# Optimization experiments

Hardware: AMD Instinct MI355X
Metric: run time of the kernel (lower is better)

The kernel has to match this reference:

```python
import jax, jax.numpy as jnp
import numpy as np

EPS = 1e-5

def conv3x3(x, w, b=None):
    # NCHW, OIHW, stride 1, padding 1
    y = jax.lax.conv_general_dilated(x, w, (1, 1), ((1, 1), (1, 1)),
                                     dimension_numbers=('NCHW', 'OIHW', 'NCHW'))
    if b is not None:
        y = y + b[None, :, None, None]
    return y

def batchnorm(x, g, b):
    # training-mode BN (PyTorch default): biased variance over (N,H,W)
    m = x.mean((0, 2, 3), keepdims=True)
    v = x.var((0, 2, 3), keepdims=True)
    return (x - m) * jax.lax.rsqrt(v + EPS) * g[None, :, None, None] + b[None, :, None, None]

def upsample2x_align_corners(x):
    # bilinear, align_corners=True, scale_factor=2
    def lerp_axis(a, Lin, axis):
        Lout = 2 * Lin
        c = jnp.arange(Lout, dtype=a.dtype) * (Lin - 1) / (Lout - 1)
        i0 = jnp.floor(c).astype(jnp.int32)
        i1 = jnp.minimum(i0 + 1, Lin - 1)
        w = c - i0.astype(a.dtype)
        shape = [1] * a.ndim
        shape[axis] = Lout
        w = w.reshape(shape)
        return jnp.take(a, i0, axis=axis) * (1 - w) + jnp.take(a, i1, axis=axis) * w
    x = lerp_axis(x, x.shape[2], 2)
    x = lerp_axis(x, x.shape[3], 3)
    return x

def deform_sample(x, offsets):
    # torchvision DeformConv2d v1 sampling: kernel 3x3, pad 1, offsets [B,18,H,W]
    # layout: per kernel point k (row-major), channels (2k, 2k+1) = (dy, dx)
    B, C, H, W = x.shape
    K = 9
    off = offsets.reshape(B, K, 2, H, W)
    ky, kx = jnp.meshgrid(jnp.arange(3) - 1, jnp.arange(3) - 1, indexing='ij')
    ky = ky.reshape(K).astype(x.dtype)
    kx = kx.reshape(K).astype(x.dtype)
    gy = jnp.arange(H, dtype=x.dtype)[None, None, :, None]
    gx = jnp.arange(W, dtype=x.dtype)[None, None, None, :]
    py = gy + ky[None, :, None, None] + off[:, :, 0]  # [B,K,H,W]
    px = gx + kx[None, :, None, None] + off[:, :, 1]
    y0 = jnp.floor(py)
    x0 = jnp.floor(px)
    wy = (py - y0)[:, None]  # [B,1,K,H,W]
    wx = (px - x0)[:, None]
    y0i = y0.astype(jnp.int32)
    x0i = x0.astype(jnp.int32)
    x_flat = x.reshape(B, C, H * W)
    def gather(yi, xi):
        valid = ((yi >= 0) & (yi < H) & (xi >= 0) & (xi < W))
        idx = jnp.clip(yi, 0, H - 1) * W + jnp.clip(xi, 0, W - 1)  # [B,K,H,W]
        g = jnp.take_along_axis(x_flat, idx.reshape(B, 1, K * H * W), axis=2)
        return g.reshape(B, C, K, H, W) * valid[:, None].astype(x.dtype)
    v00 = gather(y0i, x0i)
    v01 = gather(y0i, x0i + 1)
    v10 = gather(y0i + 1, x0i)
    v11 = gather(y0i + 1, x0i + 1)
    return (v00 * (1 - wy) * (1 - wx) + v01 * (1 - wy) * wx
            + v10 * wy * (1 - wx) + v11 * wy * wx)

def setup_inputs() -> dict:
    key = jax.random.key(0)
    ks = jax.random.split(key, 6)
    B, in_ch, skip_ch, out_ch = 4, 256, 128, 128
    Hs, Ws = 128, 128
    x = jax.random.normal(ks[0], (B, in_ch, Hs // 2, Ws // 2), jnp.float32)
    skip = jax.random.normal(ks[1], (B, skip_ch, Hs, Ws), jnp.float32)
    cat_ch = in_ch + skip_ch
    conv1_w = jax.random.normal(ks[2], (out_ch, cat_ch, 3, 3), jnp.float32) * (2.0 / (cat_ch * 9)) ** 0.5
    off_w = jax.random.normal(ks[3], (18, out_ch, 3, 3), jnp.float32) * 0.01
    off_b = jnp.zeros((18,), jnp.float32)
    def_w = jax.random.normal(ks[4], (out_ch, out_ch, 3, 3), jnp.float32) * (2.0 / (out_ch * 9)) ** 0.5
    def_b = jnp.zeros((out_ch,), jnp.float32)
    return {
        'x': x, 'skip': skip,
        'conv1_w': conv1_w,
        'bn1_g': jnp.ones((out_ch,), jnp.float32), 'bn1_b': jnp.zeros((out_ch,), jnp.float32),
        'off_w': off_w, 'off_b': off_b,
        'def_w': def_w, 'def_b': def_b,
        'bn2_g': jnp.ones((out_ch,), jnp.float32), 'bn2_b': jnp.zeros((out_ch,), jnp.float32),
    }

def reference(x, skip, conv1_w, bn1_g, bn1_b, off_w, off_b, def_w, def_b, bn2_g, bn2_b):
    xu = upsample2x_align_corners(x)
    dh = skip.shape[2] - xu.shape[2]
    dw = skip.shape[3] - xu.shape[3]
    if dh != 0 or dw != 0:
        xu = jnp.pad(xu, ((0, 0), (0, 0), (dh // 2, dh - dh // 2), (dw // 2, dw - dw // 2)))
    cat = jnp.concatenate([skip, xu], axis=1)
    h = jax.nn.relu(batchnorm(conv3x3(cat, conv1_w), bn1_g, bn1_b))
    offsets = conv3x3(h, off_w, off_b)  # [B,18,H,W]
    sampled = deform_sample(h, offsets)  # [B,C,9,H,W]
    O = def_w.shape[0]
    y = jnp.einsum('ock,bckhw->bohw', def_w.reshape(O, def_w.shape[1], 9), sampled)
    y = y + def_b[None, :, None, None]
    return jax.nn.relu(batchnorm(y, bn2_g, bn2_b))
```

## Files before the change

### kernel.cpp

```cpp
#include <hip/hip_runtime.h>
#include <hip/hip_bf16.h>

typedef __hip_bfloat16 bf16;
typedef __bf16 bf16x8 __attribute__((ext_vector_type(8)));
typedef __bf16 bf16x4 __attribute__((ext_vector_type(4)));
typedef float  f32x4  __attribute__((ext_vector_type(4)));

constexpr int NB   = 4;
constexpr int H    = 128;
constexpr int W    = 128;
constexpr int HW   = H * W;
constexpr int NPIX = NB * HW;
constexpr int CCAT = 384;
constexpr int CSKIP= 128;
constexpr int CIN  = 256;
constexpr int CO   = 128;
constexpr int HS   = 64;
constexpr int WP   = 130;
constexpr int K1   = 3456;
constexpr int KD   = 1152;
constexpr int NBORD= 2 * WP + 2 * (WP - 2);
constexpr float EPS = 1e-5f;

__device__ __forceinline__ float b2f(bf16 v){ return __bfloat162float(v); }
__device__ __forceinline__ bf16  f2b(float v){ return __float2bfloat16(v); }

__device__ __forceinline__ void async_copy16(const void* g, void* s){
    __builtin_amdgcn_global_load_lds((const __attribute__((address_space(1))) void*)g,
                                     (__attribute__((address_space(3))) void*)s, 16, 0, 0);
}

__device__ __forceinline__ int swizzle_row(int raw){
    return (raw & 7) * 64 + (raw >> 3);
}

__device__ __forceinline__ void border_yx(int p, int& y, int& x){
    if (p < WP)             { y = 0;        x = p; }
    else if (p < 2 * WP)    { y = WP - 1;   x = p - WP; }
    else if (p < 2 * WP + (WP - 2)) { y = p - 2 * WP + 1;          x = 0; }
    else                    { y = p - (2 * WP + (WP - 2)) + 1;     x = WP - 1; }
}

__global__ void k_prep(float* __restrict__ sums, bf16* __restrict__ catp,
                       bf16* __restrict__ hp){
    int i = blockIdx.x * blockDim.x + threadIdx.x;
    int stride = gridDim.x * blockDim.x;
    for (int j = i; j < 512; j += stride) sums[j] = 0.f;
    const int nCat = NB * NBORD * CCAT;
    for (int j = i; j < nCat; j += stride){
        int c = j % CCAT, r = j / CCAT, p = r % NBORD, b = r / NBORD;
        int y, x; border_yx(p, y, x);
        catp[(((size_t)b * WP + y) * WP + x) * CCAT + c] = f2b(0.f);
    }
    const int nHp = NB * NBORD * CO;
    for (int j = i; j < nHp; j += stride){
        int c = j % CO, r = j / CO, p = r % NBORD, b = r / NBORD;
        int y, x; border_yx(p, y, x);
        hp[(((size_t)b * WP + y) * WP + x) * CO + c] = f2b(0.f);
    }
}

__global__ __launch_bounds__(256) void k_build_cat2(const float* __restrict__ x,
                                                    const float* __restrict__ skip,
                                                    bf16* __restrict__ catp){
    constexpr int TS = 66;
    __shared__ bf16 tile[128 * TS];
    int t  = threadIdx.x;
    int y  = blockIdx.x % H, b = blockIdx.x / H;
    int xx = t & 127, cp = t >> 7;

    float cy = (y * 63.0f) / 127.0f;
    int   y0 = (int)cy;
    int   y1 = min(y0 + 1, HS - 1);
    float wy = cy - y0;
    float cxf = (xx * 63.0f) / 127.0f;
    int   x0 = (int)cxf;
    int   x1 = min(x0 + 1, HS - 1);
    float wx = cxf - x0;

    bf16* orow = catp + (((size_t)b * WP + y + 1) * WP + 1) * CCAT;

    for (int chunk = 0; chunk < 6; chunk++){
        int cbase = chunk * 64;
        if (chunk >= 1) __syncthreads();
        if (chunk < 2){
            const float* sb = skip + ((size_t)(b * CSKIP + cbase + cp * 32) * H + y) * W;
#pragma unroll
            for (int i = 0; i < 32; i++)
                tile[xx * TS + cp * 32 + i] = f2b(sb[(size_t)i * HW + xx]);
        } else {
            int icb = (chunk - 2) * 64 + cp * 32;
            const float* xr0 = x + ((size_t)(b * CIN + icb) * HS + y0) * HS;
            const float* xr1 = x + ((size_t)(b * CIN + icb) * HS + y1) * HS;
#pragma unroll
            for (int i = 0; i < 32; i++){
                const float* r0 = xr0 + (size_t)i * HS * HS;
                const float* r1 = xr1 + (size_t)i * HS * HS;
                float v0 = r0[x0] * (1 - wx) + r0[x1] * wx;
                float v1 = r1[x0] * (1 - wx) + r1[x1] * wx;
                tile[xx * TS + cp * 32 + i] = f2b(v0 * (1 - wy) + v1 * wy);
            }
        }
        __syncthreads();
        int cc2 = (t & 31) * 2;
        int px0 = t >> 5;
#pragma unroll
        for (int pp = 0; pp < 16; pp++){
            int px = pp * 8 + px0;
            unsigned int v = *(const unsigned int*)&tile[px * TS + cc2];
            *(unsigned int*)&orow[(size_t)px * CCAT + cbase + cc2] = v;
        }
    }
}

__global__ void k_tr_all(const float* __restrict__ w1, const float* __restrict__ wo,
                         const float* __restrict__ wd,
                         bf16* __restrict__ wt1, bf16* __restrict__ wto,
                         bf16* __restrict__ wtd){
    int i = blockIdx.x * blockDim.x + threadIdx.x;
    if (i < CO * K1){
        int k = i % K1, oc = i / K1;
        int ky = k / 1152, r = k % 1152, kx = r / 384, ic = r % 384;
        wt1[i] = f2b(w1[((oc * CCAT + ic) * 3 + ky) * 3 + kx]);
        return;
    }
    i -= CO * K1;
    if (i < 32 * KD){
        int kk = i % KD, o = i / KD;
        int ky = kk / 384, r = kk % 384, kx = r >> 7, ic = r & 127;
        wto[i] = (o < 18) ? f2b(wo[((o * CO + ic) * 3 + ky) * 3 + kx]) : f2b(0.f);
        return;
    }
    i -= 32 * KD;
    if (i < CO * KD){
        int kk = i % KD, o = i / KD;
        int kp = kk >> 7, c = kk & 127;
        wtd[i] = f2b(wd[(o * CO + c) * 9 + kp]);
    }
}

__global__ __launch_bounds__(256) void k_conv1_mfma(const bf16* __restrict__ catp,
                                                    const bf16* __restrict__ wbt,
                                                    bf16* __restrict__ hp,
                                                    float* __restrict__ sums){
    __shared__ unsigned short Ab[128 * 64];
    __shared__ unsigned short Bb[128 * 64];
    __shared__ float ps[256];
    int t = threadIdx.x;
    int l = t & 63, w = t >> 6;
    int row = swizzle_row(blockIdx.x);
    int y = row & 127, b = row >> 7;

    int pr   = l >> 3;
    int koct = (l & 7) ^ pr;
    int m    = l & 15, quad = l >> 4;
    int wm   = w & 1,  wn   = w >> 1;

    f32x4 acc[4][4];
#pragma unroll
    for (int i = 0; i < 4; i++)
#pragma unroll
        for (int j = 0; j < 4; j++) acc[i][j] = f32x4{0.f, 0.f, 0.f, 0.f};

    const size_t rowStride = (size_t)WP * CCAT;
    for (int ky = 0; ky < 3; ky++){
        const bf16* Arow = catp + ((size_t)(b * WP) + y + ky) * rowStride;
        for (int kc = 0; kc < 18; kc++){
            int c0 = kc / 6, r0 = (kc % 6) * 64;
            __syncthreads();
#pragma unroll
            for (int i = 0; i < 4; i++){
                int px = w * 32 + i * 8 + pr;
                async_copy16(Arow + (size_t)(px + c0) * CCAT + r0 + koct * 8,
                             &Ab[(w * 32 + i * 8) * 64]);
            }
            int kg = ky * 1152 + kc * 64;
#pragma unroll
            for (int i = 0; i < 4; i++){
                int oc = w * 32 + i * 8 + pr;
                async_copy16(wbt + (size_t)oc * K1 + kg + koct * 8,
                             &Bb[(w * 32 + i * 8) * 64]);
            }
            __syncthreads();
            const bf16x8* ap = (const bf16x8*)Ab;
            const bf16x8* bp = (const bf16x8*)Bb;
#pragma unroll
            for (int ks = 0; ks < 2; ks++){
                bf16x8 af[4], bfr[4];
#pragma unroll
                for (int mi = 0; mi < 4; mi++){
                    int px = wm * 64 + mi * 16 + m;
                    af[mi] = ap[px * 8 + ((ks * 4 + quad) ^ (px & 7))];
                }
#pragma unroll
                for (int ni = 0; ni < 4; ni++){
                    int oc = wn * 64 + ni * 16 + m;
                    bfr[ni] = bp[oc * 8 + ((ks * 4 + quad) ^ (oc & 7))];
                }
#pragma unroll
                for (int mi = 0; mi < 4; mi++)
#pragma unroll
                    for (int ni = 0; ni < 4; ni++)
                        acc[mi][ni] = __builtin_amdgcn_mfma_f32_16x16x32_bf16(
                            af[mi], bfr[ni], acc[mi][ni], 0, 0, 0);
            }
        }
    }
    size_t obase = (((size_t)b * WP + y + 1) * WP + 1) * CO;
#pragma unroll
    for (int mi = 0; mi < 4; mi++){
        int p0 = wm * 64 + mi * 16 + quad * 4;
#pragma unroll
        for (int ni = 0; ni < 4; ni++){
            int oc = wn * 64 + ni * 16 + m;
#pragma unroll
            for (int r = 0; r < 4; r++)
                hp[obase + (size_t)(p0 + r) * CO + oc] = f2b(acc[mi][ni][r]);
        }
    }
    ps[t] = 0.f;
    __syncthreads();
#pragma unroll
    for (int ni = 0; ni < 4; ni++){
        int ch = wn * 64 + ni * 16 + m;
        float s = 0.f, q = 0.f;
#pragma unroll
        for (int mi = 0; mi < 4; mi++)
#pragma unroll
            for (int r = 0; r < 4; r++){
                float v = acc[mi][ni][r];
                s += v; q += v * v;
            }
        atomicAdd(&ps[ch], s);
        atomicAdd(&ps[128 + ch], q);
    }
    __syncthreads();
    if (t < 128){
        atomicAdd(&sums[t],       ps[t]);
        atomicAdd(&sums[128 + t], ps[128 + t]);
    }
}

__global__ __launch_bounds__(256) void k_bn_apply_pad(bf16* __restrict__ t,
                                                      const float* __restrict__ sums,
                                                      const float* __restrict__ g,
                                                      const float* __restrict__ bb){
    __shared__ float ssc[256];
    int tt = threadIdx.x;
    if (tt < 128){
        float mean = sums[tt] / (float)NPIX;
        float var  = sums[128 + tt] / (float)NPIX - mean * mean;
        float scale = g[tt] * rsqrtf(var + EPS);
        ssc[tt]       = scale;
        ssc[128 + tt] = bb[tt] - mean * scale;
    }
    __syncthreads();
    int i = blockIdx.x * 256 + tt;
    if (i >= NPIX * CO) return;
    int c = i & 127;
    int pix = i >> 7;
    int xw = pix & 127, yh = (pix >> 7) & 127, b = pix >> 14;
    size_t a = (((size_t)b * WP + yh + 1) * WP + xw + 1) * CO + c;
    float v = b2f(t[a]) * ssc[c] + ssc[128 + c];
    t[a] = f2b(v > 0.f ? v : 0.f);
}

__global__ __launch_bounds__(256) void k_conv_off_mfma(const bf16* __restrict__ hp,
                                                       const bf16* __restrict__ wob,
                                                       const float* __restrict__ off_b,
                                                       bf16* __restrict__ offs){
    __shared__ unsigned short Ab[128 * 64];
    __shared__ unsigned short Bb[32 * 64];
    int t = threadIdx.x, l = t & 63, w = t >> 6;
    int row = swizzle_row(blockIdx.x);
    int y = row & 127, b = row >> 7;
    int pr = l >> 3, koct = (l & 7) ^ pr;
    int m = l & 15, quad = l >> 4;
    int wm = w & 1, wn = w >> 1;

    f32x4 acc[4];
#pragma unroll
    for (int i = 0; i < 4; i++) acc[i] = f32x4{0.f, 0.f, 0.f, 0.f};

    const size_t rowStride = (size_t)WP * CO;
    for (int ky = 0; ky < 3; ky++){
        const bf16* Arow = hp + ((size_t)(b * WP) + y + ky) * rowStride;
        for (int kc = 0; kc < 6; kc++){
            int kx = kc >> 1, r0 = (kc & 1) * 64;
            __syncthreads();
#pragma unroll
            for (int i = 0; i < 4; i++){
                int px = w * 32 + i * 8 + pr;
                async_copy16(Arow + (size_t)(px + kx) * CO + r0 + koct * 8,
                             &Ab[(w * 32 + i * 8) * 64]);
            }
            int kg = ky * 384 + kx * 128 + r0;
            async_copy16(wob + (size_t)(w * 8 + pr) * KD + kg + koct * 8,
                         &Bb[(w * 8) * 64]);
            __syncthreads();
            const bf16x8* ap = (const bf16x8*)Ab;
            const bf16x8* bp = (const bf16x8*)Bb;
#pragma unroll
            for (int ks = 0; ks < 2; ks++){
                int oc = wn * 16 + m;
                bf16x8 bfr = bp[oc * 8 + ((ks * 4 + quad) ^ (oc & 7))];
#pragma unroll
                for (int mi = 0; mi < 4; mi++){
                    int px = wm * 64 + mi * 16 + m;
                    bf16x8 af = ap[px * 8 + ((ks * 4 + quad) ^ (px & 7))];
                    acc[mi] = __builtin_amdgcn_mfma_f32_16x16x32_bf16(af, bfr, acc[mi], 0, 0, 0);
                }
            }
        }
    }
    int oc = wn * 16 + m;
    if (oc < 18){
        float bias = off_b[oc];
        int rowpix = b * HW + y * W;
#pragma unroll
        for (int mi = 0; mi < 4; mi++){
            int p0 = wm * 64 + mi * 16 + quad * 4;
#pragma unroll
            for (int r = 0; r < 4; r++)
                offs[(size_t)(rowpix + p0 + r) * 18 + oc] = f2b(acc[mi][r] + bias);
        }
    }
}

__global__ __launch_bounds__(256) void k_deform_mfma(const bf16* __restrict__ hp,
                                                     const bf16* __restrict__ offs,
                                                     const bf16* __restrict__ wdb,
                                                     const float* __restrict__ def_b,
                                                     bf16* __restrict__ y,
                                                     float* __restrict__ sums){
    __shared__ unsigned short Ab[128 * 64];
    __shared__ unsigned short Bb[128 * 64];
    __shared__ int2   sc_yx[9 * 128];
    __shared__ float4 sc_w[9 * 128];
    __shared__ float  ps[256];

    int t = threadIdx.x, l = t & 63, w = t >> 6;
    int row = swizzle_row(blockIdx.x);
    int yrow = row & 127, b = row >> 7;
    int rowpix = b * HW + yrow * W;

    for (int idx = t; idx < 9 * 128; idx += 256){
        int kp = idx >> 7, px = idx & 127;
        float dy = b2f(offs[(size_t)(rowpix + px) * 18 + 2 * kp]);
        float dx = b2f(offs[(size_t)(rowpix + px) * 18 + 2 * kp + 1]);
        float py = yrow + (kp / 3 - 1) + dy;
        float pxx = px + (kp % 3 - 1) + dx;
        float fy = floorf(py), fx = floorf(pxx);
        float wy = py - fy, wx = pxx - fx;
        int y0 = (int)fy, x0 = (int)fx;
        bool vy0 = (y0 >= 0) && (y0 < H);
        bool vy1 = (y0 + 1 >= 0) && (y0 + 1 < H);
        bool vx0 = (x0 >= 0) && (x0 < W);
        bool vx1 = (x0 + 1 >= 0) && (x0 + 1 < W);
        int y0c = min(max(y0, 0), H - 1),     y1c = min(max(y0 + 1, 0), H - 1);
        int x0c = min(max(x0, 0), W - 1),     x1c = min(max(x0 + 1, 0), W - 1);
        sc_yx[idx] = make_int2(((y0c + 1) * WP) | (((y1c + 1) * WP) << 16),
                               (x0c + 1) | ((x1c + 1) << 16));
        sc_w[idx] = make_float4((1 - wy) * (1 - wx) * (float)(vy0 && vx0),
                                (1 - wy) * wx       * (float)(vy0 && vx1),
                                wy * (1 - wx)       * (float)(vy1 && vx0),
                                wy * wx             * (float)(vy1 && vx1));
    }
    __syncthreads();

    int pr = l >> 3, koct = (l & 7) ^ pr;
    int m = l & 15, quad = l >> 4;
    int wm = w & 1, wn = w >> 1;
    int g = l >> 4, j = l & 15;

    f32x4 acc[4][4];
#pragma unroll
    for (int i = 0; i < 4; i++)
#pragma unroll
        for (int jj = 0; jj < 4; jj++) acc[i][jj] = f32x4{0.f, 0.f, 0.f, 0.f};

    const bf16* hpb = hp + (size_t)b * WP * WP * CO;

    for (int kc = 0; kc < 18; kc++){
        int kp = kc >> 1, ch = (kc & 1) * 64;
        __syncthreads();
        int kg = kp * 128 + ch;
#pragma unroll
        for (int i = 0; i < 4; i++){
            int oc = w * 32 + i * 8 + pr;
            async_copy16(wdb + (size_t)oc * KD + kg + koct * 8,
                         &Bb[(w * 32 + i * 8) * 64]);
        }
        int cb = ch + j * 4;
#pragma unroll
        for (int p = 0; p < 8; p++){
            int px = w * 32 + g * 8 + p;
            int idx = kp * 128 + px;
            int2 yx = sc_yx[idx];
            float4 w4 = sc_w[idx];
            int r0 = yx.x & 0xffff, r1 = ((unsigned)yx.x) >> 16;
            int c0 = yx.y & 0xffff, c1 = ((unsigned)yx.y) >> 16;
            const bf16* base = hpb + cb;
            bf16x4 s00 = *(const bf16x4*)(base + (size_t)(r0 + c0) * CO);
            bf16x4 s01 = *(const bf16x4*)(base + (size_t)(r0 + c1) * CO);
            bf16x4 s10 = *(const bf16x4*)(base + (size_t)(r1 + c0) * CO);
            bf16x4 s11 = *(const bf16x4*)(base + (size_t)(r1 + c1) * CO);
            bf16x4 pv;
#pragma unroll
            for (int r = 0; r < 4; r++){
                float v = w4.x * (float)s00[r] + w4.y * (float)s01[r]
                        + w4.z * (float)s10[r] + w4.w * (float)s11[r];
                pv[r] = (__bf16)v;
            }
            int oct_sw = (j >> 1) ^ (px & 7);
            *(bf16x4*)&Ab[px * 64 + oct_sw * 8 + (j & 1) * 4] = pv;
        }
        __syncthreads();
        const bf16x8* ap = (const bf16x8*)Ab;
        const bf16x8* bp = (const bf16x8*)Bb;
#pragma unroll
        for (int ks = 0; ks < 2; ks++){
            bf16x8 af[4], bfr[4];
#pragma unroll
            for (int mi = 0; mi < 4; mi++){
                int px = wm * 64 + mi * 16 + m;
                af[mi] = ap[px * 8 + ((ks * 4 + quad) ^ (px & 7))];
            }
#pragma unroll
            for (int ni = 0; ni < 4; ni++){
                int oc = wn * 64 + ni * 16 + m;
                bfr[ni] = bp[oc * 8 + ((ks * 4 + quad) ^ (oc & 7))];
            }
#pragma unroll
            for (int mi = 0; mi < 4; mi++)
#pragma unroll
                for (int ni = 0; ni < 4; ni++)
                    acc[mi][ni] = __builtin_amdgcn_mfma_f32_16x16x32_bf16(
                        af[mi], bfr[ni], acc[mi][ni], 0, 0, 0);
        }
    }
#pragma unroll
    for (int mi = 0; mi < 4; mi++){
        int p0 = wm * 64 + mi * 16 + quad * 4;
#pragma unroll
        for (int ni = 0; ni < 4; ni++){
            int oc = wn * 64 + ni * 16 + m;
            float bias = def_b[oc];
#pragma unroll
            for (int r = 0; r < 4; r++)
                y[(size_t)(rowpix + p0 + r) * CO + oc] = f2b(acc[mi][ni][r] + bias);
        }
    }
    ps[t] = 0.f;
    __syncthreads();
#pragma unroll
    for (int ni = 0; ni < 4; ni++){
        int ch = wn * 64 + ni * 16 + m;
        float bias = def_b[ch];
        float s = 0.f, q = 0.f;
#pragma unroll
        for (int mi = 0; mi < 4; mi++)
#pragma unroll
            for (int r = 0; r < 4; r++){
                float v = acc[mi][ni][r] + bias;
                s += v; q += v * v;
            }
        atomicAdd(&ps[ch], s);
        atomicAdd(&ps[128 + ch], q);
    }
    __syncthreads();
    if (t < 128){
        atomicAdd(&sums[t],       ps[t]);
        atomicAdd(&sums[128 + t], ps[128 + t]);
    }
}

__global__ __launch_bounds__(256) void k_final(const bf16* __restrict__ yb,
                                               const float* __restrict__ sums,
                                               const float* __restrict__ g,
                                               const float* __restrict__ bb,
                                               float* __restrict__ out){
    __shared__ unsigned short tile[128 * 129];
    __shared__ float ssc[256];
    int t = threadIdx.x;
    if (t < 128){
        float mean = sums[t] / (float)NPIX;
        float var  = sums[128 + t] / (float)NPIX - mean * mean;
        float scale = g[t] * rsqrtf(var + EPS);
        ssc[t]       = scale;
        ssc[128 + t] = bb[t] - mean * scale;
    }
    int yrow = blockIdx.x % H, b = blockIdx.x / H;
    int rowbase = b * HW + yrow * W;
    const unsigned short* src = (const unsigned short*)yb;
    for (int it = 0; it < 64; it++){
        int idx = it * 256 + t;
        int c = idx & 127, px = idx >> 7;
        tile[px * 129 + c] = src[(size_t)(rowbase + px) * CO + c];
    }
    __syncthreads();
    for (int it = 0; it < 64; it++){
        int idx = it * 256 + t;
        int xw = idx & 127, o = idx >> 7;
        unsigned short u = tile[xw * 129 + o];
        float v = (float)(*(const __bf16*)&u);
        v = v * ssc[o] + ssc[128 + o];
        out[(((size_t)b * CO + o) * H + yrow) * W + xw] = v > 0.f ? v : 0.f;
    }
}

extern "C" void kernel_launch(void* const* d_in, const int* in_sizes, int n_in,
                              void* d_out, int out_size, void* d_ws, size_t ws_size,
                              hipStream_t stream){
    const float* x      = (const float*)d_in[0];
    const float* skip   = (const float*)d_in[1];
    const float* conv1w = (const float*)d_in[2];
    const float* bn1g   = (const float*)d_in[3];
    const float* bn1b   = (const float*)d_in[4];
    const float* offw   = (const float*)d_in[5];
    const float* offb   = (const float*)d_in[6];
    const float* defw   = (const float*)d_in[7];
    const float* defb   = (const float*)d_in[8];
    const float* bn2g   = (const float*)d_in[9];
    const float* bn2b   = (const float*)d_in[10];
    float* out = (float*)d_out;

    char* ws = (char*)d_ws;
    size_t off_bytes = 0;
    auto alloc = [&](size_t bytes) -> void* {
        void* p = ws + off_bytes;
        off_bytes += (bytes + 255) & ~(size_t)255;
        return p;
    };
    const size_t catp_elems = (size_t)NB * WP * WP * CCAT;
    const size_t hp_elems   = (size_t)NB * WP * WP * CO;
    bf16*  catp  = (bf16*) alloc(catp_elems * 2);
    bf16*  hp    = (bf16*) alloc(hp_elems * 2);
    bf16*  offs  = (bf16*) alloc((size_t)NPIX * 18 * 2);
    bf16*  yb    = (bf16*) alloc((size_t)NPIX * CO * 2);
    bf16*  wbt   = (bf16*) alloc((size_t)CO * K1 * 2);
    bf16*  wob   = (bf16*) alloc((size_t)32 * KD * 2);
    bf16*  wdb   = (bf16*) alloc((size_t)CO * KD * 2);
    float* sums  = (float*)alloc(512 * 4);
    float* sums1 = sums;
    float* sums2 = sums + 256;

    k_prep<<<1024, 256, 0, stream>>>(sums, catp, hp);

    k_build_cat2<<<NB * H, 256, 0, stream>>>(x, skip, catp);

    const int ntr = CO * K1 + 32 * KD + CO * KD;
    k_tr_all<<<(ntr + 255) / 256, 256, 0, stream>>>(conv1w, offw, defw, wbt, wob, wdb);

    k_conv1_mfma<<<NB * H, 256, 0, stream>>>(catp, wbt, hp, sums1);

    k_bn_apply_pad<<<(NPIX * CO + 255) / 256, 256, 0, stream>>>(hp, sums1, bn1g, bn1b);

    k_conv_off_mfma<<<NB * H, 256, 0, stream>>>(hp, wob, offb, offs);

    k_deform_mfma<<<NB * H, 256, 0, stream>>>(hp, offs, wdb, defb, yb, sums2);

    k_final<<<NB * H, 256, 0, stream>>>(yb, sums2, bn2g, bn2b, out);
}
```

Before: 349.5 us.

## Process two output rows per conv1 block, drop row swizzle, shuffle-reduce BN stats

conv1 now uses 512-thread blocks that each compute two image rows (256 pixels) against a shared 128-channel weight tile. Each weight chunk is therefore loaded once for twice the pixels, and the grid is halved. The XCD-style row swizzle is removed from all kernels in favour of plain linear row mapping. BN partial sums are wave-reduced with shuffles before the LDS atomics, which cuts atomic contention. The larger LDS footprint and block size may lower occupancy, and dropping the swizzle changes cache locality across dies.

```diff
diff --git a/kernel.cpp b/kernel.cpp
--- a/kernel.cpp
+++ b/kernel.cpp
@@ -30,10 +30,6 @@
                                      (__attribute__((address_space(3))) void*)s, 16, 0, 0);
 }
 
-__device__ __forceinline__ int swizzle_row(int raw){
-    return (raw & 7) * 64 + (raw >> 3);
-}
-
 __device__ __forceinline__ void border_yx(int p, int& y, int& x){
     if (p < WP)             { y = 0;        x = p; }
     else if (p < 2 * WP)    { y = WP - 1;   x = p - WP; }
@@ -139,22 +135,21 @@
     }
 }
 
-__global__ __launch_bounds__(256) void k_conv1_mfma(const bf16* __restrict__ catp,
+__global__ __launch_bounds__(512) void k_conv1_mfma(const bf16* __restrict__ catp,
                                                     const bf16* __restrict__ wbt,
                                                     bf16* __restrict__ hp,
                                                     float* __restrict__ sums){
-    __shared__ unsigned short Ab[128 * 64];
+    __shared__ unsigned short Ab[256 * 64];
     __shared__ unsigned short Bb[128 * 64];
     __shared__ float ps[256];
     int t = threadIdx.x;
     int l = t & 63, w = t >> 6;
-    int row = swizzle_row(blockIdx.x);
-    int y = row & 127, b = row >> 7;
+    int y0 = (blockIdx.x & 63) * 2, b = blockIdx.x >> 6;
 
     int pr   = l >> 3;
     int koct = (l & 7) ^ pr;
     int m    = l & 15, quad = l >> 4;
-    int wm   = w & 1,  wn   = w >> 1;
+    int wm   = w & 3,  wn   = w >> 2;
 
     f32x4 acc[4][4];
 #pragma unroll
@@ -163,23 +158,27 @@
         for (int j = 0; j < 4; j++) acc[i][j] = f32x4{0.f, 0.f, 0.f, 0.f};
 
     const size_t rowStride = (size_t)WP * CCAT;
+    const bf16* Abase = catp + ((size_t)(b * WP) + y0) * rowStride;
+
     for (int ky = 0; ky < 3; ky++){
-        const bf16* Arow = catp + ((size_t)(b * WP) + y + ky) * rowStride;
         for (int kc = 0; kc < 18; kc++){
             int c0 = kc / 6, r0 = (kc % 6) * 64;
             __syncthreads();
 #pragma unroll
             for (int i = 0; i < 4; i++){
-                int px = w * 32 + i * 8 + pr;
-                async_copy16(Arow + (size_t)(px + c0) * CCAT + r0 + koct * 8,
-                             &Ab[(w * 32 + i * 8) * 64]);
+                int pxg = i * 64 + w * 8;
+                int rr  = pxg >> 7;
+                int xl  = (pxg & 127) + pr;
+                const bf16* Arow = Abase + (size_t)(rr + ky) * rowStride;
+                async_copy16(Arow + (size_t)(xl + c0) * CCAT + r0 + koct * 8,
+                             &Ab[pxg * 64]);
             }
             int kg = ky * 1152 + kc * 64;
 #pragma unroll
-            for (int i = 0; i < 4; i++){
-                int oc = w * 32 + i * 8 + pr;
-                async_copy16(wbt + (size_t)oc * K1 + kg + koct * 8,
-                             &Bb[(w * 32 + i * 8) * 64]);
+            for (int i = 0; i < 2; i++){
+                int ocg = i * 64 + w * 8;
+                async_copy16(wbt + (size_t)(ocg + pr) * K1 + kg + koct * 8,
+                             &Bb[ocg * 64]);
             }
             __syncthreads();
             const bf16x8* ap = (const bf16x8*)Ab;
@@ -206,19 +205,19 @@
             }
         }
     }
-    size_t obase = (((size_t)b * WP + y + 1) * WP + 1) * CO;
 #pragma unroll
     for (int mi = 0; mi < 4; mi++){
         int p0 = wm * 64 + mi * 16 + quad * 4;
+        size_t obase = (((size_t)b * WP + y0 + (p0 >> 7) + 1) * WP + 1 + (p0 & 127)) * CO;
 #pragma unroll
         for (int ni = 0; ni < 4; ni++){
             int oc = wn * 64 + ni * 16 + m;
 #pragma unroll
             for (int r = 0; r < 4; r++)
-                hp[obase + (size_t)(p0 + r) * CO + oc] = f2b(acc[mi][ni][r]);
-        }
-    }
-    ps[t] = 0.f;
+                hp[obase + (size_t)r * CO + oc] = f2b(acc[mi][ni][r]);
+        }
+    }
+    if (t < 256) ps[t] = 0.f;
     __syncthreads();
 #pragma unroll
     for (int ni = 0; ni < 4; ni++){
@@ -231,8 +230,12 @@
                 float v = acc[mi][ni][r];
                 s += v; q += v * v;
             }
-        atomicAdd(&ps[ch], s);
-        atomicAdd(&ps[128 + ch], q);
+        s += __shfl_xor(s, 16); s += __shfl_xor(s, 32);
+        q += __shfl_xor(q, 16); q += __shfl_xor(q, 32);
+        if (quad == 0){
+            atomicAdd(&ps[ch], s);
+            atomicAdd(&ps[128 + ch], q);
+        }
     }
     __syncthreads();
     if (t < 128){
@@ -272,8 +275,7 @@
     __shared__ unsigned short Ab[128 * 64];
     __shared__ unsigned short Bb[32 * 64];
     int t = threadIdx.x, l = t & 63, w = t >> 6;
-    int row = swizzle_row(blockIdx.x);
-    int y = row & 127, b = row >> 7;
+    int y = blockIdx.x % H, b = blockIdx.x / H;
     int pr = l >> 3, koct = (l & 7) ^ pr;
     int m = l & 15, quad = l >> 4;
     int wm = w & 1, wn = w >> 1;
@@ -340,8 +342,7 @@
     __shared__ float  ps[256];
 
     int t = threadIdx.x, l = t & 63, w = t >> 6;
-    int row = swizzle_row(blockIdx.x);
-    int yrow = row & 127, b = row >> 7;
+    int yrow = blockIdx.x % H, b = blockIdx.x / H;
     int rowpix = b * HW + yrow * W;
 
     for (int idx = t; idx < 9 * 128; idx += 256){
@@ -465,8 +466,12 @@
                 float v = acc[mi][ni][r] + bias;
                 s += v; q += v * v;
             }
-        atomicAdd(&ps[ch], s);
-        atomicAdd(&ps[128 + ch], q);
+        s += __shfl_xor(s, 16); s += __shfl_xor(s, 32);
+        q += __shfl_xor(q, 16); q += __shfl_xor(q, 32);
+        if (quad == 0){
+            atomicAdd(&ps[ch], s);
+            atomicAdd(&ps[128 + ch], q);
+        }
     }
     __syncthreads();
     if (t < 128){
@@ -552,7 +557,7 @@
     const int ntr = CO * K1 + 32 * KD + CO * KD;
     k_tr_all<<<(ntr + 255) / 256, 256, 0, stream>>>(conv1w, offw, defw, wbt, wob, wdb);
 
-    k_conv1_mfma<<<NB * H, 256, 0, stream>>>(catp, wbt, hp, sums1);
+    k_conv1_mfma<<<NB * H / 2, 512, 0, stream>>>(catp, wbt, hp, sums1);
 
     k_bn_apply_pad<<<(NPIX * CO + 255) / 256, 256, 0, stream>>>(hp, sums1, bn1g, bn1b);
 
```

Measured after the change: 359.3 us. 2.8% more time.
